# Performance work log

Hardware: AMD Instinct MI355X
Metric: run time of the kernel (lower is better)

## Reference

```python
import jax, jax.numpy as jnp
import numpy as np


def setup_inputs() -> dict:
    key = jax.random.key(0)
    k1, k2, k3 = jax.random.split(key, 3)
    B, H, W, D, K = 16, 32, 32, 128, 32
    x = jax.random.normal(k1, (B, H, W, D), dtype=jnp.float32)
    std = 1.0 / (K * D) ** 0.5
    codewords = jax.random.uniform(k2, (K, D), minval=-std, maxval=std, dtype=jnp.float32)
    scale = jax.random.uniform(k3, (K,), minval=-1.0, maxval=0.0, dtype=jnp.float32)
    return {"x": x, "codewords": codewords, "scale": scale}


def reference(x, codewords, scale):
    B, H, W, D = x.shape
    K = codewords.shape[0]
    X = x.reshape(B, H * W, D)                      # [B, N, D]
    # scaled squared distances: s_k * ||x_n - c_k||^2 via expansion (no BNKD tensor)
    x2 = jnp.sum(X * X, axis=-1, keepdims=True)     # [B, N, 1]
    c2 = jnp.sum(codewords * codewords, axis=-1)    # [K]
    xc = jnp.einsum('bnd,kd->bnk', X, codewords)    # [B, N, K]
    SL = scale[None, None, :] * (x2 - 2.0 * xc + c2[None, None, :])
    A = jax.nn.softmax(SL, axis=2)                  # assignment weights [B, N, K]
    # E_bk = sum_n A_bnk * (x_bn - c_k)
    E = jnp.einsum('bnk,bnd->bkd', A, X) - jnp.sum(A, axis=1)[:, :, None] * codewords[None]
    return E
```

## Files before the change

kernel.cpp:

```cpp
#include <hip/hip_runtime.h>


typedef __attribute__((ext_vector_type(8))) short bf16x8;
typedef __attribute__((ext_vector_type(16))) float f32x16;

constexpr int XBS = 136;
constexpr int AST = 40;

__device__ __forceinline__ unsigned short f2bf(float f) {
    unsigned u = __float_as_uint(f);
    u += 0x7fffu + ((u >> 16) & 1u);
    return (unsigned short)(u >> 16);
}
__device__ __forceinline__ float bf2f(unsigned short h) {
    return __uint_as_float((unsigned)h << 16);
}

__global__ __launch_bounds__(256)
void enc_partial(const float* __restrict__ x, const float* __restrict__ cw,
                 const float* __restrict__ scale, unsigned short* __restrict__ ws)
{
    __shared__ unsigned short xb_s[32 * XBS];
    __shared__ unsigned short cb_s[32 * XBS];
    __shared__ unsigned short At_s[32 * AST];
    __shared__ float x2_s[32], c2_s[32];
    __shared__ float asum_s[4 * 32];
    __shared__ float asumf_s[32];

    const int tid = threadIdx.x;
    const int b   = blockIdx.x >> 5;
    const int s   = blockIdx.x & 31;
    const int lc  = tid & 31;
    const int lh  = (tid >> 5) & 1;
    const int w   = tid >> 6;

    const float4* xg4 = (const float4*)(x + (size_t)(b * 1024 + s * 32) * 128);
    const float4* cg4 = (const float4*)cw;

#pragma unroll
    for (int i = 0; i < 4; ++i) {
        const int f   = tid + 256 * i;
        const int row = 8 * i + (tid >> 5);
        const int col = tid & 31;
        float4 vx = xg4[f];
        float4 vc = cg4[f];
        short4 hx = { (short)f2bf(vx.x), (short)f2bf(vx.y),
                      (short)f2bf(vx.z), (short)f2bf(vx.w) };
        short4 hc = { (short)f2bf(vc.x), (short)f2bf(vc.y),
                      (short)f2bf(vc.z), (short)f2bf(vc.w) };
        *(short4*)&xb_s[row * XBS + col * 4] = hx;
        *(short4*)&cb_s[row * XBS + col * 4] = hc;
        float sx = vx.x * vx.x + vx.y * vx.y + vx.z * vx.z + vx.w * vx.w;
        float sc = vc.x * vc.x + vc.y * vc.y + vc.z * vc.z + vc.w * vc.w;
#pragma unroll
        for (int m = 16; m >= 1; m >>= 1) {
            sx += __shfl_xor(sx, m);
            sc += __shfl_xor(sc, m);
        }
        if (col == 0) { x2_s[row] = sx; c2_s[row] = sc; }
    }
    __syncthreads();

    f32x16 acc;
#pragma unroll
    for (int i = 0; i < 16; ++i) acc[i] = 0.f;
#pragma unroll
    for (int t = 0; t < 8; ++t) {
        bf16x8 af  = *(const bf16x8*)&xb_s[lc * XBS + t * 16 + lh * 8];
        bf16x8 bfr = *(const bf16x8*)&cb_s[lc * XBS + t * 16 + lh * 8];
        acc = __builtin_amdgcn_mfma_f32_32x32x16_bf16(af, bfr, acc, 0, 0, 0);
    }

    {
        const float sck = scale[lc];
        const float c2k = c2_s[lc];
        const float4 x2v = *(const float4*)&x2_s[8 * w + 4 * lh];
        float sl[4] = {
            sck * (x2v.x - 2.f * acc[4 * w + 0] + c2k),
            sck * (x2v.y - 2.f * acc[4 * w + 1] + c2k),
            sck * (x2v.z - 2.f * acc[4 * w + 2] + c2k),
            sck * (x2v.w - 2.f * acc[4 * w + 3] + c2k) };
        float a[4];
#pragma unroll
        for (int q = 0; q < 4; ++q) {
            float m = sl[q];
#pragma unroll
            for (int msk = 16; msk >= 1; msk >>= 1) m = fmaxf(m, __shfl_xor(m, msk));
            float e = __expf(sl[q] - m);
            float den = e;
#pragma unroll
            for (int msk = 16; msk >= 1; msk >>= 1) den += __shfl_xor(den, msk);
            a[q] = e / den;
        }
        short4 ha = { (short)f2bf(a[0]), (short)f2bf(a[1]),
                      (short)f2bf(a[2]), (short)f2bf(a[3]) };
        *(short4*)&At_s[lc * AST + 8 * w + 4 * lh] = ha;
        float ap = (a[0] + a[1]) + (a[2] + a[3]);
        ap += __shfl_xor(ap, 32);
        if (lh == 0) asum_s[w * 32 + lc] = ap;
    }
    __syncthreads();

    if (tid < 32)
        asumf_s[tid] = (asum_s[tid] + asum_s[32 + tid]) +
                       (asum_s[64 + tid] + asum_s[96 + tid]);

    f32x16 e;
#pragma unroll
    for (int i = 0; i < 16; ++i) e[i] = 0.f;
#pragma unroll
    for (int t = 0; t < 2; ++t) {
        bf16x8 af = *(const bf16x8*)&At_s[lc * AST + t * 16 + lh * 8];
        const int nb = t * 16 + lh * 8;
        bf16x8 bfr;
#pragma unroll
        for (int j = 0; j < 8; ++j)
            bfr[j] = (short)xb_s[(nb + j) * XBS + w * 32 + lc];
        e = __builtin_amdgcn_mfma_f32_32x32x16_bf16(af, bfr, e, 0, 0, 0);
    }
    __syncthreads();

    {
        unsigned short* wb = ws + (size_t)(b * 32 + s) * 4096;
        const int dd = w * 32 + lc;
#pragma unroll
        for (int r = 0; r < 16; ++r) {
            const int kk = (r & 3) + 8 * (r >> 2) + 4 * lh;
            float v = e[r] - asumf_s[kk] * bf2f(cb_s[kk * XBS + dd]);
            wb[kk * 128 + dd] = f2bf(v);
        }
    }
}

__global__ __launch_bounds__(256)
void enc_reduce(const unsigned short* __restrict__ ws, float* __restrict__ out)
{
    __shared__ float red_s[3][256];

    const int tid  = threadIdx.x;
    const int lane = tid & 63;
    const int sg   = tid >> 6;
    const int b    = blockIdx.x >> 4;
    const int q    = (blockIdx.x & 15) * 64 + lane;
    const unsigned short* base = ws + (size_t)b * 131072 + q * 4;

    float4 a0 = {0,0,0,0}, a1 = {0,0,0,0};
#pragma unroll
    for (int s = 0; s < 8; s += 2) {
        ushort4 v0 = *(const ushort4*)&base[(sg * 8 + s + 0) * 4096];
        ushort4 v1 = *(const ushort4*)&base[(sg * 8 + s + 1) * 4096];
        a0.x += bf2f(v0.x); a0.y += bf2f(v0.y); a0.z += bf2f(v0.z); a0.w += bf2f(v0.w);
        a1.x += bf2f(v1.x); a1.y += bf2f(v1.y); a1.z += bf2f(v1.z); a1.w += bf2f(v1.w);
    }
    float4 a;
    a.x = a0.x + a1.x; a.y = a0.y + a1.y; a.z = a0.z + a1.z; a.w = a0.w + a1.w;

    if (sg) *(float4*)&red_s[sg - 1][lane * 4] = a;
    __syncthreads();
    if (sg == 0) {
        float4 r0 = *(const float4*)&red_s[0][lane * 4];
        float4 r1 = *(const float4*)&red_s[1][lane * 4];
        float4 r2 = *(const float4*)&red_s[2][lane * 4];
        float4 r;
        r.x = (a.x + r0.x) + (r1.x + r2.x);
        r.y = (a.y + r0.y) + (r1.y + r2.y);
        r.z = (a.z + r0.z) + (r1.z + r2.z);
        r.w = (a.w + r0.w) + (r1.w + r2.w);
        *(float4*)&out[(size_t)b * 4096 + q * 4] = r;
    }
}

extern "C" void kernel_launch(void* const* d_in, const int* in_sizes, int n_in,
                              void* d_out, int out_size, void* d_ws, size_t ws_size,
                              hipStream_t stream)
{
    const float* x     = (const float*)d_in[0];
    const float* cw    = (const float*)d_in[1];
    const float* scale = (const float*)d_in[2];
    float* out = (float*)d_out;
    unsigned short* ws = (unsigned short*)d_ws;

    enc_partial<<<512, 256, 0, stream>>>(x, cw, scale, ws);
    enc_reduce<<<256, 256, 0, stream>>>(ws, out);
}
```

Measured before the change: 67.17 us.

## Process 64 rows per block to halve partial sums and workspace traffic

Each block of the partial kernel now handles 64 spatial positions instead of 32. Wave pairs split the distance GEMM across two 32-row halves, and the aggregation MFMA loops over 64 rows. This halves the number of blocks and the bf16 partial-sum workspace that the reduce kernel reads, and amortizes the per-block codeword staging. The cost is fewer blocks, 256 for 256 CUs, and more per-block work and shared memory, which lowers occupancy and latency hiding.

```diff
diff --git a/kernel.cpp b/kernel.cpp
--- a/kernel.cpp
+++ b/kernel.cpp
@@ -5,7 +5,7 @@
 typedef __attribute__((ext_vector_type(16))) float f32x16;
 
 constexpr int XBS = 136;
-constexpr int AST = 40;
+constexpr int AST = 72;
 
 __device__ __forceinline__ unsigned short f2bf(float f) {
     unsigned u = __float_as_uint(f);
@@ -20,44 +20,52 @@
 void enc_partial(const float* __restrict__ x, const float* __restrict__ cw,
                  const float* __restrict__ scale, unsigned short* __restrict__ ws)
 {
-    __shared__ unsigned short xb_s[32 * XBS];
+    __shared__ unsigned short xb_s[64 * XBS];
     __shared__ unsigned short cb_s[32 * XBS];
     __shared__ unsigned short At_s[32 * AST];
-    __shared__ float x2_s[32], c2_s[32];
+    __shared__ float x2_s[64], c2_s[32];
     __shared__ float asum_s[4 * 32];
     __shared__ float asumf_s[32];
 
     const int tid = threadIdx.x;
-    const int b   = blockIdx.x >> 5;
-    const int s   = blockIdx.x & 31;
+    const int b   = blockIdx.x >> 4;
+    const int s   = blockIdx.x & 15;
     const int lc  = tid & 31;
     const int lh  = (tid >> 5) & 1;
     const int w   = tid >> 6;
+    const int g   = w >> 1;
+    const int p   = w & 1;
 
-    const float4* xg4 = (const float4*)(x + (size_t)(b * 1024 + s * 32) * 128);
+    const float4* xg4 = (const float4*)(x + (size_t)(b * 1024 + s * 64) * 128);
     const float4* cg4 = (const float4*)cw;
 
+#pragma unroll
+    for (int i = 0; i < 8; ++i) {
+        const int f   = tid + 256 * i;
+        const int row = 8 * i + (tid >> 5);
+        const int col = tid & 31;
+        float4 vx = xg4[f];
+        short4 hx = { (short)f2bf(vx.x), (short)f2bf(vx.y),
+                      (short)f2bf(vx.z), (short)f2bf(vx.w) };
+        *(short4*)&xb_s[row * XBS + col * 4] = hx;
+        float sx = vx.x * vx.x + vx.y * vx.y + vx.z * vx.z + vx.w * vx.w;
+#pragma unroll
+        for (int m = 16; m >= 1; m >>= 1) sx += __shfl_xor(sx, m);
+        if (col == 0) x2_s[row] = sx;
+    }
 #pragma unroll
     for (int i = 0; i < 4; ++i) {
         const int f   = tid + 256 * i;
         const int row = 8 * i + (tid >> 5);
         const int col = tid & 31;
-        float4 vx = xg4[f];
         float4 vc = cg4[f];
-        short4 hx = { (short)f2bf(vx.x), (short)f2bf(vx.y),
-                      (short)f2bf(vx.z), (short)f2bf(vx.w) };
         short4 hc = { (short)f2bf(vc.x), (short)f2bf(vc.y),
                       (short)f2bf(vc.z), (short)f2bf(vc.w) };
-        *(short4*)&xb_s[row * XBS + col * 4] = hx;
         *(short4*)&cb_s[row * XBS + col * 4] = hc;
-        float sx = vx.x * vx.x + vx.y * vx.y + vx.z * vx.z + vx.w * vx.w;
         float sc = vc.x * vc.x + vc.y * vc.y + vc.z * vc.z + vc.w * vc.w;
 #pragma unroll
-        for (int m = 16; m >= 1; m >>= 1) {
-            sx += __shfl_xor(sx, m);
-            sc += __shfl_xor(sc, m);
-        }
-        if (col == 0) { x2_s[row] = sx; c2_s[row] = sc; }
+        for (int m = 16; m >= 1; m >>= 1) sc += __shfl_xor(sc, m);
+        if (col == 0) c2_s[row] = sc;
     }
     __syncthreads();
 
@@ -66,7 +74,7 @@
     for (int i = 0; i < 16; ++i) acc[i] = 0.f;
 #pragma unroll
     for (int t = 0; t < 8; ++t) {
-        bf16x8 af  = *(const bf16x8*)&xb_s[lc * XBS + t * 16 + lh * 8];
+        bf16x8 af  = *(const bf16x8*)&xb_s[(32 * g + lc) * XBS + t * 16 + lh * 8];
         bf16x8 bfr = *(const bf16x8*)&cb_s[lc * XBS + t * 16 + lh * 8];
         acc = __builtin_amdgcn_mfma_f32_32x32x16_bf16(af, bfr, acc, 0, 0, 0);
     }
@@ -74,30 +82,36 @@
     {
         const float sck = scale[lc];
         const float c2k = c2_s[lc];
-        const float4 x2v = *(const float4*)&x2_s[8 * w + 4 * lh];
-        float sl[4] = {
-            sck * (x2v.x - 2.f * acc[4 * w + 0] + c2k),
-            sck * (x2v.y - 2.f * acc[4 * w + 1] + c2k),
-            sck * (x2v.z - 2.f * acc[4 * w + 2] + c2k),
-            sck * (x2v.w - 2.f * acc[4 * w + 3] + c2k) };
-        float a[4];
+        float asum8 = 0.f;
 #pragma unroll
-        for (int q = 0; q < 4; ++q) {
-            float m = sl[q];
+        for (int j = 0; j < 2; ++j) {
+            const int nb = 32 * g + 16 * p + 8 * j + 4 * lh;
+            const float4 x2v = *(const float4*)&x2_s[nb];
+            const int rb = 8 * p + 4 * j;
+            float sl[4] = {
+                sck * (x2v.x - 2.f * acc[rb + 0] + c2k),
+                sck * (x2v.y - 2.f * acc[rb + 1] + c2k),
+                sck * (x2v.z - 2.f * acc[rb + 2] + c2k),
+                sck * (x2v.w - 2.f * acc[rb + 3] + c2k) };
+            float a[4];
 #pragma unroll
-            for (int msk = 16; msk >= 1; msk >>= 1) m = fmaxf(m, __shfl_xor(m, msk));
-            float e = __expf(sl[q] - m);
-            float den = e;
+            for (int q = 0; q < 4; ++q) {
+                float m = sl[q];
 #pragma unroll
-            for (int msk = 16; msk >= 1; msk >>= 1) den += __shfl_xor(den, msk);
-            a[q] = e / den;
+                for (int msk = 16; msk >= 1; msk >>= 1) m = fmaxf(m, __shfl_xor(m, msk));
+                float e = __expf(sl[q] - m);
+                float den = e;
+#pragma unroll
+                for (int msk = 16; msk >= 1; msk >>= 1) den += __shfl_xor(den, msk);
+                a[q] = e / den;
+            }
+            short4 ha = { (short)f2bf(a[0]), (short)f2bf(a[1]),
+                          (short)f2bf(a[2]), (short)f2bf(a[3]) };
+            *(short4*)&At_s[lc * AST + nb] = ha;
+            asum8 += (a[0] + a[1]) + (a[2] + a[3]);
         }
-        short4 ha = { (short)f2bf(a[0]), (short)f2bf(a[1]),
-                      (short)f2bf(a[2]), (short)f2bf(a[3]) };
-        *(short4*)&At_s[lc * AST + 8 * w + 4 * lh] = ha;
-        float ap = (a[0] + a[1]) + (a[2] + a[3]);
-        ap += __shfl_xor(ap, 32);
-        if (lh == 0) asum_s[w * 32 + lc] = ap;
+        asum8 += __shfl_xor(asum8, 32);
+        if (lh == 0) asum_s[w * 32 + lc] = asum8;
     }
     __syncthreads();
 
@@ -109,7 +123,7 @@
 #pragma unroll
     for (int i = 0; i < 16; ++i) e[i] = 0.f;
 #pragma unroll
-    for (int t = 0; t < 2; ++t) {
+    for (int t = 0; t < 4; ++t) {
         bf16x8 af = *(const bf16x8*)&At_s[lc * AST + t * 16 + lh * 8];
         const int nb = t * 16 + lh * 8;
         bf16x8 bfr;
@@ -121,7 +135,7 @@
     __syncthreads();
 
     {
-        unsigned short* wb = ws + (size_t)(b * 32 + s) * 4096;
+        unsigned short* wb = ws + (size_t)(b * 16 + s) * 4096;
         const int dd = w * 32 + lc;
 #pragma unroll
         for (int r = 0; r < 16; ++r) {
@@ -142,13 +156,13 @@
     const int sg   = tid >> 6;
     const int b    = blockIdx.x >> 4;
     const int q    = (blockIdx.x & 15) * 64 + lane;
-    const unsigned short* base = ws + (size_t)b * 131072 + q * 4;
+    const unsigned short* base = ws + (size_t)b * 65536 + q * 4;
 
     float4 a0 = {0,0,0,0}, a1 = {0,0,0,0};
 #pragma unroll
-    for (int s = 0; s < 8; s += 2) {
-        ushort4 v0 = *(const ushort4*)&base[(sg * 8 + s + 0) * 4096];
-        ushort4 v1 = *(const ushort4*)&base[(sg * 8 + s + 1) * 4096];
+    for (int s = 0; s < 4; s += 2) {
+        ushort4 v0 = *(const ushort4*)&base[(sg * 4 + s + 0) * 4096];
+        ushort4 v1 = *(const ushort4*)&base[(sg * 4 + s + 1) * 4096];
         a0.x += bf2f(v0.x); a0.y += bf2f(v0.y); a0.z += bf2f(v0.z); a0.w += bf2f(v0.w);
         a1.x += bf2f(v1.x); a1.y += bf2f(v1.y); a1.z += bf2f(v1.z); a1.w += bf2f(v1.w);
     }
@@ -180,6 +194,6 @@
     float* out = (float*)d_out;
     unsigned short* ws = (unsigned short*)d_ws;
 
-    enc_partial<<<512, 256, 0, stream>>>(x, cw, scale, ws);
+    enc_partial<<<256, 256, 0, stream>>>(x, cw, scale, ws);
     enc_reduce<<<256, 256, 0, stream>>>(ws, out);
 }
```

After: 69.48 us. +3.4%, slower.
